# Performance work log

Hardware: AMD Instinct MI355X
Metric: run time of the kernel (lower is better)

The kernel has to match this reference:

```python
import jax, jax.numpy as jnp
import numpy as np

N_EMBD = 1024
N_HEAD = 16
HEAD_DIM = N_EMBD // N_HEAD


def setup_inputs() -> dict:
    key = jax.random.key(0)
    ks = jax.random.split(key, 5)
    B, T, C = 2, 2048, N_EMBD
    scale = 0.02
    return {
        "x": jax.random.normal(ks[0], (B, T, C), dtype=jnp.float32),
        "w_attn": jax.random.normal(ks[1], (C, 3 * C), dtype=jnp.float32) * scale,
        "b_attn": jax.random.normal(ks[2], (3 * C,), dtype=jnp.float32) * scale,
        "w_proj": jax.random.normal(ks[3], (C, C), dtype=jnp.float32) * scale,
        "b_proj": jax.random.normal(ks[4], (C,), dtype=jnp.float32) * scale,
    }


def reference(x, w_attn, b_attn, w_proj, b_proj):
    B, T, C = x.shape
    H, D = N_HEAD, HEAD_DIM
    qkv = x @ w_attn + b_attn  # [B,T,3C]
    q, k, v = jnp.split(qkv, 3, axis=-1)
    # [B,T,C] -> [B,H,T,D]
    q = q.reshape(B, T, H, D).transpose(0, 2, 1, 3)
    k = k.reshape(B, T, H, D).transpose(0, 2, 1, 3)
    v = v.reshape(B, T, H, D).transpose(0, 2, 1, 3)
    scores = jnp.einsum("bhqd,bhkd->bhqk", q, k) / jnp.sqrt(jnp.float32(D))
    causal = jnp.tril(jnp.ones((T, T), dtype=bool))
    scores = jnp.where(causal, scores, jnp.finfo(scores.dtype).min)
    attn = jax.nn.softmax(scores, axis=-1)
    y = jnp.einsum("bhqk,bhkd->bhqd", attn, v)  # [B,H,T,D]
    y = y.transpose(0, 2, 1, 3).reshape(B, T, C)
    return y @ w_proj + b_proj
```

## Files before the change

### kernel.cpp

```cpp
#include <hip/hip_runtime.h>

typedef unsigned short u16;
typedef u16 u16x4 __attribute__((ext_vector_type(4)));
typedef u16 u16x8 __attribute__((ext_vector_type(8)));
typedef __bf16 bf16x8 __attribute__((ext_vector_type(8)));
typedef float floatx4 __attribute__((ext_vector_type(4)));

#define N_EMBD 1024
#define N_HEAD 16
#define HEAD_DIM 64
#define SEQ 2048
#define BATCH 2
#define M_ROWS (BATCH * SEQ)

typedef __attribute__((address_space(1))) const unsigned char ga_t;
typedef __attribute__((address_space(3))) unsigned char la_t;

#if __has_builtin(__builtin_amdgcn_exp2f)
#define EXP2(x) __builtin_amdgcn_exp2f(x)
#else
#define EXP2(x) exp2f(x)
#endif

__device__ __forceinline__ u16 cvt_bf16(float f) {
  return __builtin_bit_cast(u16, (__bf16)f);
}

__global__ __launch_bounds__(256) void prep(const float* __restrict__ x,
                                            u16* __restrict__ xb,
                                            const float* __restrict__ wa,
                                            const float* __restrict__ wp,
                                            u16* __restrict__ outa,
                                            u16* __restrict__ outp) {
  const int bid = blockIdx.x;
  if (bid < 2048) {
    const long i = ((long)bid * 256 + threadIdx.x) * 8;
    const float4 f0 = *(const float4*)&x[i];
    const float4 f1 = *(const float4*)&x[i + 4];
    u16x8 p;
    p[0] = cvt_bf16(f0.x); p[1] = cvt_bf16(f0.y);
    p[2] = cvt_bf16(f0.z); p[3] = cvt_bf16(f0.w);
    p[4] = cvt_bf16(f1.x); p[5] = cvt_bf16(f1.y);
    p[6] = cvt_bf16(f1.z); p[7] = cvt_bf16(f1.w);
    *(u16x8*)&xb[i] = p;
    return;
  }
  __shared__ u16 tile[32][33];
  const int t = bid - 2048;
  const int gx = t & 127;
  const int gy = t >> 7;
  const int R = N_EMBD;
  const float* in;
  u16* out;
  int C, bx;
  if (gx < 96) {
    in = wa; out = outa; C = 3 * N_EMBD; bx = gx * 32;
  } else {
    in = wp; out = outp; C = N_EMBD; bx = (gx - 96) * 32;
  }
  const int by = gy * 32;
  const int tx = threadIdx.x & 31;
  const int ty = threadIdx.x >> 5;
#pragma unroll
  for (int j = 0; j < 32; j += 8)
    tile[ty + j][tx] = cvt_bf16(in[(long)(by + ty + j) * C + bx + tx]);
  __syncthreads();
#pragma unroll
  for (int j = 0; j < 32; j += 8)
    out[(long)(bx + ty + j) * R + by + tx] = tile[tx][ty + j];
}

#define BK 32

template <int MODE>
__device__ __forceinline__ void stage128(const u16* __restrict__ A,
                                         const u16* __restrict__ Bt, int bm,
                                         int bn, int kt, int K, int tid,
                                         u16* as, u16* bs) {
  const int w = tid >> 6;
  const int l = tid & 63;
  const int lrow = l >> 2;
#pragma unroll
  for (int p = 0; p < 2; ++p) {
    const int arow = p * 64 + w * 16;
    const int row = arow + lrow;
    const int sl = (l & 3) ^ ((row >> 1) & 3);
    long gA;
    if (MODE == 0) {
      gA = (long)(bm + row) * K + kt + sl * 8;
    } else {
      const int m = bm + row;
      const int b = m >> 11, t = m & 2047;
      const int k0 = kt + sl * 8;
      const int head = k0 >> 6, dd = k0 & 63;
      gA = (((long)(b * N_HEAD + head)) * SEQ + t) * HEAD_DIM + dd;
    }
    __builtin_amdgcn_global_load_lds((ga_t*)(A + gA), (la_t*)&as[arow * BK],
                                     16, 0, 0);
  }
  constexpr int TN = (MODE == 1) ? 64 : 128;
#pragma unroll
  for (int p = 0; p < TN / 64; ++p) {
    const int arow = p * 64 + w * 16;
    const int row = arow + lrow;
    const int sl = (l & 3) ^ ((row >> 1) & 3);
    const long gB = (long)(bn + row) * K + kt + sl * 8;
    __builtin_amdgcn_global_load_lds((ga_t*)(Bt + gB), (la_t*)&bs[arow * BK],
                                     16, 0, 0);
  }
}

template <int MODE>
__global__ __launch_bounds__(256) void gemm128(
    const u16* __restrict__ A, const u16* __restrict__ Bt,
    const float* __restrict__ bias, float* __restrict__ out,
    u16* __restrict__ qo, u16* __restrict__ ko, u16* __restrict__ vo, int N,
    int K) {
  constexpr int TN = (MODE == 1) ? 64 : 128;
  constexpr int NJ = TN / 32;
  __shared__ u16 As[2][128 * BK];
  __shared__ u16 Bs[2][TN * BK];
  const int tid = threadIdx.x;

  const int nx = gridDim.x;
  const int nwg = nx * gridDim.y;
  int lin = blockIdx.y * nx + blockIdx.x;
  lin = (lin & 7) * (nwg >> 3) + (lin >> 3);
  const int bm = (lin / nx) * 128;
  const int bn = (lin % nx) * TN;

  const int w = tid >> 6;
  const int l = tid & 63;
  const int wm = (w >> 1) * 64;
  const int wn = (w & 1) * (TN / 2);
  const int m16 = l & 15;
  const int quad = l >> 4;
  const int ksw = (quad ^ ((m16 >> 1) & 3)) * 8;

  floatx4 acc[4][NJ];
#pragma unroll
  for (int i = 0; i < 4; ++i)
#pragma unroll
    for (int j = 0; j < NJ; ++j) acc[i][j] = (floatx4){0.f, 0.f, 0.f, 0.f};

  const int nk = K / BK;
  stage128<MODE>(A, Bt, bm, bn, 0, K, tid, As[0], Bs[0]);

  int cur = 0;
  for (int t = 0; t < nk; ++t) {
    if (t + 1 < nk) {
      stage128<MODE>(A, Bt, bm, bn, (t + 1) * BK, K, tid, As[cur ^ 1],
                     Bs[cur ^ 1]);
      if constexpr (MODE == 0)
        asm volatile("s_waitcnt vmcnt(4)" ::: "memory");
      else
        asm volatile("s_waitcnt vmcnt(3)" ::: "memory");
    } else {
      asm volatile("s_waitcnt vmcnt(0)" ::: "memory");
    }
    __builtin_amdgcn_s_barrier();

    bf16x8 af[4], bfr[NJ];
#pragma unroll
    for (int i = 0; i < 4; ++i)
      af[i] = __builtin_bit_cast(
          bf16x8, *(const u16x8*)&As[cur][(wm + i * 16 + m16) * BK + ksw]);
#pragma unroll
    for (int j = 0; j < NJ; ++j)
      bfr[j] = __builtin_bit_cast(
          bf16x8, *(const u16x8*)&Bs[cur][(wn + j * 16 + m16) * BK + ksw]);
#pragma unroll
    for (int i = 0; i < 4; ++i)
#pragma unroll
      for (int j = 0; j < NJ; ++j)
        acc[i][j] = __builtin_amdgcn_mfma_f32_16x16x32_bf16(af[i], bfr[j],
                                                            acc[i][j], 0, 0, 0);
    __builtin_amdgcn_s_barrier();
    cur ^= 1;
  }

#pragma unroll
  for (int i = 0; i < 4; ++i) {
#pragma unroll
    for (int j = 0; j < NJ; ++j) {
      const int col = bn + wn + j * 16 + m16;
      const float bv = bias[col];
      if (MODE == 1) {
#pragma unroll
        for (int r = 0; r < 4; ++r) {
          const int row = bm + wm + i * 16 + quad * 4 + r;
          out[(long)row * N_EMBD + col] = acc[i][j][r] + bv;
        }
      } else {
        const int which = col >> 10;
        const int cc = col & 1023;
        const int h = cc >> 6;
        const int dd = cc & 63;
        const int row0 = bm + wm + i * 16 + quad * 4;
        const int b = row0 >> 11;
        const int t0 = row0 & 2047;
        if (which == 2) {
          u16x4 pk;
#pragma unroll
          for (int r = 0; r < 4; ++r) pk[r] = cvt_bf16(acc[i][j][r] + bv);
          *(u16x4*)&vo[(((long)(b * N_HEAD + h)) * HEAD_DIM + dd) * SEQ + t0] =
              pk;
        } else {
          u16* dst = (which == 0) ? qo : ko;
#pragma unroll
          for (int r = 0; r < 4; ++r)
            dst[(((long)(b * N_HEAD + h)) * SEQ + t0 + r) * HEAD_DIM + dd] =
                cvt_bf16(acc[i][j][r] + bv);
        }
      }
    }
  }
}

#define BQ 64
#define BKV 64
#define LOG2E 1.44269504f
#define NQT (SEQ / BQ)
#define NROWS (32 * SEQ)

__device__ __forceinline__ void stage_kv(const u16* __restrict__ K,
                                         const u16* __restrict__ Vt, long bh,
                                         int kt, int tid, u16* kl, u16* vl) {
#pragma unroll
  for (int i = 0; i < 2; ++i) {
    const int p = tid + 256 * i;
    const int row = p >> 3;
    const int slot = (p & 7) ^ (row & 7);
    const int wb = (i * 256 + (tid & 192)) * 8;
    __builtin_amdgcn_global_load_lds(
        (ga_t*)&K[(bh * SEQ + kt + row) * HEAD_DIM + slot * 8], (la_t*)&kl[wb],
        16, 0, 0);
    __builtin_amdgcn_global_load_lds(
        (ga_t*)&Vt[(bh * HEAD_DIM + row) * SEQ + kt + slot * 8], (la_t*)&vl[wb],
        16, 0, 0);
  }
}

__global__ __launch_bounds__(256, 4) void flash_attn(
    const u16* __restrict__ Qy, const u16* __restrict__ K,
    const u16* __restrict__ Vt, float* __restrict__ Opart,
    float2* __restrict__ mlpart) {
  const int id = blockIdx.x;
  const int a = id >> 6;
  const int h = (id >> 5) & 1;
  const long bh = id & 31;
  const int tid = threadIdx.x;
  const int w = tid >> 6;
  const int l = tid & 63;
  const int m16 = l & 15;
  const int quad = l >> 4;

  __shared__ u16 Kl[2][BKV * 64];
  __shared__ u16 Vl[2][64 * BKV];
  __shared__ u16 Pl[4][16 * 64];

  const float SC = 0.125f * LOG2E;
  const int sw = (m16 & 7) << 3;

  for (int ph = 0; ph < 2; ++ph) {
    const int iq = ph ? (31 - a) : a;
    const int na = iq + 1;
    const int mid = (na + 1) >> 1;
    const int s0 = h ? mid : 0;
    const int e0 = h ? na : mid;
    const int qglob = iq * BQ + w * 16 + m16;

    bf16x8 qf[2];
    {
      const u16* qrow = Qy + (bh * SEQ + qglob) * HEAD_DIM;
      qf[0] = __builtin_bit_cast(bf16x8, *(const u16x8*)&qrow[quad * 8]);
      qf[1] = __builtin_bit_cast(bf16x8, *(const u16x8*)&qrow[32 + quad * 8]);
    }

    floatx4 Oacc[4];
#pragma unroll
    for (int t = 0; t < 4; ++t) Oacc[t] = (floatx4){0.f, 0.f, 0.f, 0.f};
    float mrow = -1e30f, lsum = 0.f;

    if (s0 < e0) {
      stage_kv(K, Vt, bh, s0 * BKV, tid, Kl[0], Vl[0]);
      __syncthreads();

      for (int it = s0; it < e0; ++it) {
        const int buf = (it - s0) & 1;
        const int kt = it * BKV;
        if (it + 1 < e0)
          stage_kv(K, Vt, bh, kt + BKV, tid, Kl[buf ^ 1], Vl[buf ^ 1]);

        floatx4 s[4];
#pragma unroll
        for (int j = 0; j < 4; ++j) s[j] = (floatx4){0.f, 0.f, 0.f, 0.f};
#pragma unroll
        for (int j = 0; j < 4; ++j)
#pragma unroll
          for (int kk = 0; kk < 2; ++kk) {
            const bf16x8 kf = __builtin_bit_cast(
                bf16x8, *(const u16x8*)&Kl[buf][(j * 16 + m16) * 64 +
                                                ((kk * 32 + quad * 8) ^ sw)]);
            s[j] = __builtin_amdgcn_mfma_f32_16x16x32_bf16(kf, qf[kk], s[j], 0,
                                                           0, 0);
          }
        if (it == na - 1) {
#pragma unroll
          for (int j = 0; j < 4; ++j) {
            const int key0 = kt + j * 16 + quad * 4;
#pragma unroll
            for (int r = 0; r < 4; ++r)
              if (key0 + r > qglob) s[j][r] = -1e30f;
          }
        }

        float t0 = fmaxf(fmaxf(s[0][0], s[0][1]), fmaxf(s[0][2], s[0][3]));
        float t1 = fmaxf(fmaxf(s[1][0], s[1][1]), fmaxf(s[1][2], s[1][3]));
        float t2 = fmaxf(fmaxf(s[2][0], s[2][1]), fmaxf(s[2][2], s[2][3]));
        float t3 = fmaxf(fmaxf(s[3][0], s[3][1]), fmaxf(s[3][2], s[3][3]));
        float tm = fmaxf(fmaxf(t0, t1), fmaxf(t2, t3));
        tm = fmaxf(tm, __shfl_xor(tm, 16, 64));
        tm = fmaxf(tm, __shfl_xor(tm, 32, 64));
        const float pm = tm * SC;
        if (!__all(pm <= mrow + 4.f)) {
          const float mn = fmaxf(mrow, pm);
          const float al = EXP2(mrow - mn);
          mrow = mn;
          lsum *= al;
#pragma unroll
          for (int t = 0; t < 4; ++t)
#pragma unroll
            for (int r = 0; r < 4; ++r) Oacc[t][r] *= al;
        }

        float ls = 0.f;
#pragma unroll
        for (int j = 0; j < 4; ++j) {
          u16x4 pk;
#pragma unroll
          for (int r = 0; r < 4; ++r) {
            const float p = EXP2(__builtin_fmaf(s[j][r], SC, -mrow));
            ls += p;
            pk[r] = cvt_bf16(p);
          }
          *(u16x4*)&Pl[w][m16 * 64 + ((j * 16 + quad * 4) ^ sw)] = pk;
        }
        lsum += ls;

        bf16x8 pf[2];
        pf[0] = __builtin_bit_cast(
            bf16x8, *(const u16x8*)&Pl[w][m16 * 64 + ((quad * 8) ^ sw)]);
        pf[1] = __builtin_bit_cast(
            bf16x8, *(const u16x8*)&Pl[w][m16 * 64 + ((32 + quad * 8) ^ sw)]);
#pragma unroll
        for (int t = 0; t < 4; ++t)
#pragma unroll
          for (int kk = 0; kk < 2; ++kk) {
            const bf16x8 vf = __builtin_bit_cast(
                bf16x8, *(const u16x8*)&Vl[buf][(t * 16 + m16) * 64 +
                                                ((kk * 32 + quad * 8) ^ sw)]);
            Oacc[t] = __builtin_amdgcn_mfma_f32_16x16x32_bf16(vf, pf[kk],
                                                              Oacc[t], 0, 0, 0);
          }
        __syncthreads();
      }
    }

    float lt = lsum;
    lt += __shfl_xor(lt, 16, 64);
    lt += __shfl_xor(lt, 32, 64);
    const long row = bh * SEQ + qglob;
    float* Op = Opart + (long)h * NROWS * HEAD_DIM;
#pragma unroll
    for (int t = 0; t < 4; ++t)
      *(floatx4*)&Op[row * HEAD_DIM + t * 16 + quad * 4] = Oacc[t];
    if (quad == 0) mlpart[h * NROWS + row] = make_float2(mrow, lt);
  }
}

__global__ __launch_bounds__(256) void merge_attn(
    const float* __restrict__ Opart, const float2* __restrict__ mlpart,
    u16* __restrict__ Qy) {
  const int bid = blockIdx.x;
  const int bh = (bid & 7) | (((bid >> 10) & 3) << 3);
  const int chunk = (bid >> 3) & 127;
  const int r = threadIdx.x >> 4;
  const int d0 = (threadIdx.x & 15) * 4;
  const long row = (long)bh * SEQ + chunk * 16 + r;
  const float2 A = mlpart[row];
  const float2 B = mlpart[NROWS + row];
  const float M = fmaxf(A.x, B.x);
  const float w0 = EXP2(A.x - M), w1 = EXP2(B.x - M);
  const float inv = 1.f / (w0 * A.y + w1 * B.y);
  const floatx4 o0 = *(const floatx4*)&Opart[row * HEAD_DIM + d0];
  const floatx4 o1 =
      *(const floatx4*)&Opart[(long)NROWS * HEAD_DIM + row * HEAD_DIM + d0];
  u16x4 pk;
#pragma unroll
  for (int i = 0; i < 4; ++i)
    pk[i] = cvt_bf16((w0 * o0[i] + w1 * o1[i]) * inv);
  *(u16x4*)&Qy[row * HEAD_DIM + d0] = pk;
}

extern "C" void kernel_launch(void* const* d_in, const int* in_sizes, int n_in,
                              void* d_out, int out_size, void* d_ws,
                              size_t ws_size, hipStream_t stream) {
  const float* x = (const float*)d_in[0];
  const float* w_attn = (const float*)d_in[1];
  const float* b_attn = (const float*)d_in[2];
  const float* w_proj = (const float*)d_in[3];
  const float* b_proj = (const float*)d_in[4];
  float* out = (float*)d_out;

  char* ws = (char*)d_ws;
  const size_t SZ = (size_t)BATCH * N_HEAD * SEQ * HEAD_DIM * sizeof(u16);
  u16* q = (u16*)(ws);
  u16* k = (u16*)(ws + SZ);
  u16* vT = (u16*)(ws + 2 * SZ);
  u16* wT_a = (u16*)(ws + 3 * SZ);
  u16* wT_p = (u16*)(ws + 3 * SZ + (size_t)3 * N_EMBD * N_EMBD * sizeof(u16));
  u16* xb = (u16*)(ws + 3 * SZ + (size_t)4 * N_EMBD * N_EMBD * sizeof(u16));
  float* Opart = (float*)(ws + (size_t)48 * 1024 * 1024);
  float2* mlpart =
      (float2*)(ws + (size_t)48 * 1024 * 1024 +
                (size_t)2 * NROWS * HEAD_DIM * sizeof(float));

  prep<<<2048 + 4096, 256, 0, stream>>>(x, xb, w_attn, w_proj, wT_a, wT_p);

  gemm128<0><<<dim3(3 * N_EMBD / 128, M_ROWS / 128), 256, 0, stream>>>(
      xb, wT_a, b_attn, nullptr, q, k, vT, 3 * N_EMBD, N_EMBD);

  flash_attn<<<1024, 256, 0, stream>>>(q, k, vT, Opart, mlpart);

  merge_attn<<<4096, 256, 0, stream>>>(Opart, mlpart, q);

  gemm128<1><<<dim3(N_EMBD / 64, M_ROWS / 128), 256, 0, stream>>>(
      q, wT_p, b_proj, out, nullptr, nullptr, nullptr, N_EMBD, N_EMBD);
}
```

Baseline: 176.8 us.

## Triple-buffer GEMM LDS staging and raise wave priority around attention MFMAs

```diff
diff --git a/kernel.cpp b/kernel.cpp
--- a/kernel.cpp
+++ b/kernel.cpp
@@ -118,8 +118,8 @@
     int K) {
   constexpr int TN = (MODE == 1) ? 64 : 128;
   constexpr int NJ = TN / 32;
-  __shared__ u16 As[2][128 * BK];
-  __shared__ u16 Bs[2][TN * BK];
+  __shared__ u16 As[3][128 * BK];
+  __shared__ u16 Bs[3][TN * BK];
   const int tid = threadIdx.x;
 
   const int nx = gridDim.x;
@@ -145,12 +145,13 @@
 
   const int nk = K / BK;
   stage128<MODE>(A, Bt, bm, bn, 0, K, tid, As[0], Bs[0]);
-
-  int cur = 0;
+  stage128<MODE>(A, Bt, bm, bn, BK, K, tid, As[1], Bs[1]);
+
+  u16 *a0 = As[0], *a1 = As[1], *a2 = As[2];
+  u16 *b0 = Bs[0], *b1 = Bs[1], *b2 = Bs[2];
+
   for (int t = 0; t < nk; ++t) {
     if (t + 1 < nk) {
-      stage128<MODE>(A, Bt, bm, bn, (t + 1) * BK, K, tid, As[cur ^ 1],
-                     Bs[cur ^ 1]);
       if constexpr (MODE == 0)
         asm volatile("s_waitcnt vmcnt(4)" ::: "memory");
       else
@@ -160,23 +161,26 @@
     }
     __builtin_amdgcn_s_barrier();
 
+    if (t + 2 < nk)
+      stage128<MODE>(A, Bt, bm, bn, (t + 2) * BK, K, tid, a2, b2);
+
     bf16x8 af[4], bfr[NJ];
 #pragma unroll
     for (int i = 0; i < 4; ++i)
       af[i] = __builtin_bit_cast(
-          bf16x8, *(const u16x8*)&As[cur][(wm + i * 16 + m16) * BK + ksw]);
+          bf16x8, *(const u16x8*)&a0[(wm + i * 16 + m16) * BK + ksw]);
 #pragma unroll
     for (int j = 0; j < NJ; ++j)
       bfr[j] = __builtin_bit_cast(
-          bf16x8, *(const u16x8*)&Bs[cur][(wn + j * 16 + m16) * BK + ksw]);
+          bf16x8, *(const u16x8*)&b0[(wn + j * 16 + m16) * BK + ksw]);
 #pragma unroll
     for (int i = 0; i < 4; ++i)
 #pragma unroll
       for (int j = 0; j < NJ; ++j)
         acc[i][j] = __builtin_amdgcn_mfma_f32_16x16x32_bf16(af[i], bfr[j],
                                                             acc[i][j], 0, 0, 0);
-    __builtin_amdgcn_s_barrier();
-    cur ^= 1;
+    u16* ta = a0; a0 = a1; a1 = a2; a2 = ta;
+    u16* tb = b0; b0 = b1; b1 = b2; b2 = tb;
   }
 
 #pragma unroll
@@ -295,6 +299,7 @@
         floatx4 s[4];
 #pragma unroll
         for (int j = 0; j < 4; ++j) s[j] = (floatx4){0.f, 0.f, 0.f, 0.f};
+        __builtin_amdgcn_s_setprio(1);
 #pragma unroll
         for (int j = 0; j < 4; ++j)
 #pragma unroll
@@ -305,6 +310,7 @@
             s[j] = __builtin_amdgcn_mfma_f32_16x16x32_bf16(kf, qf[kk], s[j], 0,
                                                            0, 0);
           }
+        __builtin_amdgcn_s_setprio(0);
         if (it == na - 1) {
 #pragma unroll
           for (int j = 0; j < 4; ++j) {
@@ -315,11 +321,12 @@
           }
         }
 
-        float t0 = fmaxf(fmaxf(s[0][0], s[0][1]), fmaxf(s[0][2], s[0][3]));
-        float t1 = fmaxf(fmaxf(s[1][0], s[1][1]), fmaxf(s[1][2], s[1][3]));
-        float t2 = fmaxf(fmaxf(s[2][0], s[2][1]), fmaxf(s[2][2], s[2][3]));
-        float t3 = fmaxf(fmaxf(s[3][0], s[3][1]), fmaxf(s[3][2], s[3][3]));
-        float tm = fmaxf(fmaxf(t0, t1), fmaxf(t2, t3));
+        float tm = s[0][0];
+#pragma unroll
+        for (int j = 0; j < 4; ++j)
+#pragma unroll
+          for (int r = 0; r < 4; ++r)
+            if (j + r) tm = fmaxf(tm, s[j][r]);
         tm = fmaxf(tm, __shfl_xor(tm, 16, 64));
         tm = fmaxf(tm, __shfl_xor(tm, 32, 64));
         const float pm = tm * SC;
@@ -353,6 +360,7 @@
             bf16x8, *(const u16x8*)&Pl[w][m16 * 64 + ((quad * 8) ^ sw)]);
         pf[1] = __builtin_bit_cast(
             bf16x8, *(const u16x8*)&Pl[w][m16 * 64 + ((32 + quad * 8) ^ sw)]);
+        __builtin_amdgcn_s_setprio(1);
 #pragma unroll
         for (int t = 0; t < 4; ++t)
 #pragma unroll
@@ -363,6 +371,7 @@
             Oacc[t] = __builtin_amdgcn_mfma_f32_16x16x32_bf16(vf, pf[kk],
                                                               Oacc[t], 0, 0, 0);
           }
+        __builtin_amdgcn_s_setprio(0);
         __syncthreads();
       }
     }
```

Result: no change. 178.5 us (+0.9%).
